# Optimization experiments

Hardware: AMD Instinct MI355X
Metric: run time of the kernel (lower is better)

Reference implementation:

```python
import jax, jax.numpy as jnp
import numpy as np

N = 50000      # nodes
E = 800000     # edges (avg degree 16)
C = 32         # channels per degree (deg0 and deg1)
HRAD = 32      # radial MLP hidden
L = 4          # attention layers (plus 1 output layer)
HEADS = 4
EPS = 1e-6
NRAD = 7 * C   # rk00, rk10, rv00, rv10, rv11, rv01, rv11b


def setup_inputs() -> dict:
    key = jax.random.key(0)
    ks = jax.random.split(key, 16)
    L1 = L + 1
    s = 0.1
    return {
        "pos": jax.random.normal(ks[0], (N, 3), jnp.float32),
        "f0": jax.random.normal(ks[1], (N, C), jnp.float32),
        "f1": jax.random.normal(ks[2], (N, C, 3), jnp.float32),
        "src": jax.random.randint(ks[3], (E,), 0, N, jnp.int32),
        "dst": jax.random.randint(ks[4], (E,), 0, N, jnp.int32),
        "W1": jax.random.normal(ks[5], (L1, 1, HRAD), jnp.float32) * s,
        "b1": jnp.zeros((L1, HRAD), jnp.float32),
        "W2": jax.random.normal(ks[6], (L1, HRAD, NRAD), jnp.float32) * s,
        "b2": jnp.zeros((L1, NRAD), jnp.float32),
        "Wq": jax.random.normal(ks[7], (L1, C, C), jnp.float32) * s,
        "Wo0": jax.random.normal(ks[8], (L1, C, C), jnp.float32) * s,
        "Wo1": jax.random.normal(ks[9], (L1, C, C), jnp.float32) * s,
        "Ws0": jax.random.normal(ks[10], (L1, C, C), jnp.float32) * s,
        "Ws1": jax.random.normal(ks[11], (L1, C, C), jnp.float32) * s,
        "bg": jnp.zeros((L, C), jnp.float32),
    }


def _attn_layer(f0, f1, u, rlen, src, dst, n, heads,
                W1, b1, W2, b2, Wq, Wo0, Wo1, Ws0, Ws1):
    # radial network, channel-wise modulation per interaction path
    h = jax.nn.relu(rlen[:, None] @ W1 + b1)            # [E, HRAD]
    R = h @ W2 + b2                                     # [E, 7C]
    rk00, rk10, rv00, rv10, rv11, rv01, rv11b = jnp.split(R, 7, axis=-1)
    f0s = f0[src]                                       # [E, C]
    f1s = f1[src]                                       # [E, C, 3]
    dot1 = jnp.einsum('ecd,ed->ec', f1s, u)             # deg1 -> invariant [E, C]
    # equivariant keys (deg0) and values (deg0 + deg1)
    k0 = rk00 * f0s + rk10 * dot1                       # [E, C]
    v0 = rv00 * f0s + rv10 * dot1                       # [E, C]
    v1 = rv11[..., None] * f1s + (rv01 * f0s + rv11b * dot1)[..., None] * u[:, None, :]  # [E, C, 3]
    # multi-head attention logits on invariants
    ch = C // heads
    q = (f0 @ Wq)[dst].reshape(-1, heads, ch)           # [E, H, ch]
    kh = k0.reshape(-1, heads, ch)
    logits = (q * kh).sum(-1) / np.sqrt(ch)             # [E, H]
    # segment softmax over incoming edges of each dst node
    m = jax.ops.segment_max(logits, dst, num_segments=n)
    e = jnp.exp(logits - m[dst])
    z = jax.ops.segment_sum(e, dst, num_segments=n)
    alpha = e / (z[dst] + EPS)                          # [E, H]
    ac = jnp.repeat(alpha, ch, axis=1)                  # [E, C]
    o0 = jax.ops.segment_sum(ac * v0, dst, num_segments=n)                  # [N, C]
    o1 = jax.ops.segment_sum(ac[..., None] * v1, dst, num_segments=n)       # [N, C, 3]
    # self-interaction + skip
    out0 = o0 @ Wo0 + f0 @ Ws0
    out1 = jnp.einsum('ncd,ce->ned', o1, Wo1) + jnp.einsum('ncd,ce->ned', f1, Ws1)
    return out0, out1


def _forward(pos, f0, f1, src, dst, W1, b1, W2, b2, Wq, Wo0, Wo1, Ws0, Ws1, bg):
    n = f0.shape[0]
    # edge-wise basis (l=0,1 spherical harmonics ~ unit direction) and radial distance
    rel = pos[dst] - pos[src]                           # [E, 3]
    rlen = jnp.linalg.norm(rel, axis=-1)                # [E]
    u = rel / (rlen + EPS)[:, None]                     # [E, 3]
    for i in range(L):
        f0, f1 = _attn_layer(f0, f1, u, rlen, src, dst, n, HEADS,
                             W1[i], b1[i], W2[i], b2[i], Wq[i],
                             Wo0[i], Wo1[i], Ws0[i], Ws1[i])
        # GProjRelu: relu on invariants, norm-gated relu on deg-1
        f0 = jax.nn.relu(f0)
        n1 = jnp.linalg.norm(f1, axis=-1)               # [N, C]
        f1 = f1 * (jax.nn.relu(n1 + bg[i]) / (n1 + EPS))[..., None]
    # final output layer: single head, no nonlinearity
    f0, f1 = _attn_layer(f0, f1, u, rlen, src, dst, n, 1,
                         W1[L], b1[L], W2[L], b2[L], Wq[L],
                         Wo0[L], Wo1[L], Ws0[L], Ws1[L])
    return f0, f1


def reference(pos, f0, f1, src, dst, W1, b1, W2, b2, Wq, Wo0, Wo1, Ws0, Ws1, bg):
    return _forward(pos, f0, f1, src, dst, W1, b1, W2, b2, Wq, Wo0, Wo1, Ws0, Ws1, bg)
```

## Files before the change

### kernel.cpp

```cpp
#include <hip/hip_runtime.h>
#include <math.h>

#define CCH 32
#define NCH 224
#define NIV 33
#define HRAD 32
#define ET 16


__global__ void hist_kernel(const int* __restrict__ dst, int* __restrict__ counts, int E) {
  int e = blockIdx.x * 256 + threadIdx.x;
  if (e < E) atomicAdd(&counts[dst[e]], 1);
}

__global__ void scan1_kernel(const int* __restrict__ counts, int* __restrict__ offs,
                             int* __restrict__ bsums, int n) {
  __shared__ int sd[1024];
  int t = threadIdx.x;
  int i = blockIdx.x * 1024 + t;
  int v = (i < n) ? counts[i] : 0;
  sd[t] = v;
  __syncthreads();
  for (int o = 1; o < 1024; o <<= 1) {
    int add = (t >= o) ? sd[t - o] : 0;
    __syncthreads();
    sd[t] += add;
    __syncthreads();
  }
  if (i < n) offs[i] = sd[t] - v;
  if (t == 1023) bsums[blockIdx.x] = sd[1023];
}

__global__ void scan2_kernel(int* bsums, int nb) {
  if (threadIdx.x == 0 && blockIdx.x == 0) {
    int acc = 0;
    for (int i = 0; i < nb; i++) { int v = bsums[i]; bsums[i] = acc; acc += v; }
  }
}

__global__ void scan3_kernel(int* __restrict__ offs, const int* __restrict__ bsums,
                             int* __restrict__ cursor, int n, int E) {
  int i = blockIdx.x * 256 + threadIdx.x;
  if (i < n) {
    int v = offs[i] + bsums[i >> 10];
    offs[i] = v;
    cursor[i] = v;
  } else if (i == n) {
    offs[n] = E;
  }
}

__global__ void scatter_kernel(const float* __restrict__ pos, const int* __restrict__ src,
                               const int* __restrict__ dst, int* __restrict__ cursor,
                               int* __restrict__ esrcS, float4* __restrict__ egeoS, int E) {
  int e = blockIdx.x * 256 + threadIdx.x;
  if (e >= E) return;
  int s = src[e], d = dst[e];
  float rx = pos[d * 3 + 0] - pos[s * 3 + 0];
  float ry = pos[d * 3 + 1] - pos[s * 3 + 1];
  float rz = pos[d * 3 + 2] - pos[s * 3 + 2];
  float rl = sqrtf(rx * rx + ry * ry + rz * rz);
  float inv = 1.0f / (rl + 1e-6f);
  int p = atomicAdd(&cursor[d], 1);
  esrcS[p] = s;
  egeoS[p] = make_float4(rx * inv, ry * inv, rz * inv, rl);
}


__global__ void pwl_build_kernel(const float* __restrict__ W1, const float* __restrict__ b1,
                                 const float* __restrict__ W2, const float* __restrict__ b2,
                                 float2* __restrict__ coef, float* __restrict__ tks) {
  int l = blockIdx.x;
  int tid = threadIdx.x;
  const float* w1 = W1 + l * HRAD;
  const float* bb1 = b1 + l * HRAD;
  const float* w2 = W2 + l * HRAD * NCH;
  const float* bb2 = b2 + l * NCH;
  __shared__ float a_s[HRAD], b_s[HRAD], t_s[HRAD], t_sorted[HRAD];
  if (tid < HRAD) {
    float a = w1[tid], b = bb1[tid];
    a_s[tid] = a; b_s[tid] = b;
    t_s[tid] = (a != 0.0f) ? (-b / a) : 1e30f;
  }
  __syncthreads();
  if (tid < HRAD) {
    float tj = t_s[tid];
    int rank = 0;
    for (int k = 0; k < HRAD; k++) {
      float tk = t_s[k];
      rank += (tk < tj) || (tk == tj && k < tid);
    }
    t_sorted[rank] = tj;
    tks[l * HRAD + tid] = tj;
  }
  __syncthreads();
  for (int idx = tid; idx < NIV * NCH; idx += blockDim.x) {
    int iv = idx / NCH;
    int k = idx - iv * NCH;
    double lo = (iv == 0) ? (double)t_sorted[0] - 1.0 : (double)t_sorted[iv - 1];
    double hi = (iv == NIV - 1) ? (double)t_sorted[HRAD - 1] + 1.0 : (double)t_sorted[iv];
    double rm = 0.5 * (lo + hi);
    if (iv == 0) rm = (double)t_sorted[0] - 1.0;
    if (iv == NIV - 1) rm = (double)t_sorted[HRAD - 1] + 1.0;
    float alpha = bb2[k];
    float beta = 0.0f;
    for (int j = 0; j < HRAD; j++) {
      if ((double)a_s[j] * rm + (double)b_s[j] > 0.0) {
        float w = w2[j * NCH + k];
        alpha = fmaf(w, b_s[j], alpha);
        beta = fmaf(w, a_s[j], beta);
      }
    }
    coef[l * (NIV * NCH) + idx] = make_float2(alpha, beta);
  }
}


__global__ __launch_bounds__(512) void pack_kernel(
    const float* __restrict__ f0, const float* __restrict__ f1,
    const float* __restrict__ Wq0, float scale0,
    float4* __restrict__ fpk, float* __restrict__ qbuf, int n) {
  __shared__ float sWq[1024];
  __shared__ float sF0[ET * 32];
  int tid = threadIdx.x;
  for (int i = tid; i < 1024; i += 512) sWq[i] = Wq0[i];
  __syncthreads();
  int nl = tid >> 5, c = tid & 31;
  for (int base = blockIdx.x * ET; base < n; base += gridDim.x * ET) {
    int node = base + nl;
    float v0 = 0.f, x = 0.f, y = 0.f, z = 0.f;
    if (node < n) {
      v0 = f0[(size_t)node * 32 + c];
      size_t b = ((size_t)node * 32 + c) * 3;
      x = f1[b]; y = f1[b + 1]; z = f1[b + 2];
      fpk[(size_t)node * 32 + c] = make_float4(v0, x, y, z);
    }
    sF0[nl * 32 + c] = v0;
    __syncthreads();
    if (node < n) {
      float q = 0.f;
#pragma unroll
      for (int k = 0; k < 32; k++) q = fmaf(sF0[nl * 32 + k], sWq[k * 32 + c], q);
      qbuf[(size_t)node * 32 + c] = q * scale0;
    }
    __syncthreads();
  }
}


__global__ __launch_bounds__(1024) void node_kernel(
    const float4* __restrict__ fpk, const float* __restrict__ qbuf,
    float4* __restrict__ Opk,
    const int* __restrict__ esrcS, const float4* __restrict__ egeoS,
    const int* __restrict__ offs,
    const float2* __restrict__ coefG, const float* __restrict__ tkG,
    int ch, int n) {
  __shared__ float2 sCoef[NIV * NCH];
  __shared__ float sTk[CCH];
  int tid = threadIdx.x;
  for (int i = tid; i < NIV * NCH; i += 1024) sCoef[i] = coefG[i];
  if (tid < CCH) sTk[tid] = tkG[tid];
  __syncthreads();

  int lane = tid & 63;
  int wid = tid >> 6;
  int c = lane & 31;
  int half = lane >> 5;
  float tk_c = sTk[c];

  for (int node = blockIdx.x * 16 + wid; node < n; node += gridDim.x * 16) {
    float qs = qbuf[(size_t)node * 32 + c];
    int start = offs[node], end = offs[node + 1];
    float m = -INFINITY, z = 0.0f;
    float o0 = 0.0f, o10 = 0.0f, o11 = 0.0f, o12 = 0.0f;

    int j = start + half;
    int sB = 0;
    float4 gA = make_float4(0, 0, 0, 0), gB = make_float4(0, 0, 0, 0);
    float4 FA = make_float4(0, 0, 0, 0);
    if (j < end) {
      int sA = esrcS[j];
      gA = egeoS[j];
      FA = fpk[(size_t)sA * 32 + c];
    }
    if (j + 2 < end) { sB = esrcS[j + 2]; gB = egeoS[j + 2]; }

    while (j < end) {
      float4 g = gA;
      float4 F = FA;
      int j2 = j + 2;
      if (j2 < end) {
        FA = fpk[(size_t)sB * 32 + c];
        gA = gB;
        if (j2 + 2 < end) { sB = esrcS[j2 + 2]; gB = egeoS[j2 + 2]; }
      }
      unsigned long long msk = __ballot(g.w > tk_c);
      int iv = half ? (int)__popcll(msk >> 32) : (int)__popcll(msk & 0xFFFFFFFFull);
      const float2* cf = sCoef + iv * NCH + c;
      float r = g.w;
      float2 q0 = cf[0],   q1 = cf[32],  q2 = cf[64], q3 = cf[96];
      float2 q4 = cf[128], q5 = cf[160], q6 = cf[192];
      float rk00 = fmaf(q0.y, r, q0.x), rk10 = fmaf(q1.y, r, q1.x);
      float rv00 = fmaf(q2.y, r, q2.x), rv10 = fmaf(q3.y, r, q3.x);
      float rv11 = fmaf(q4.y, r, q4.x), rv01 = fmaf(q5.y, r, q5.x);
      float rv11b = fmaf(q6.y, r, q6.x);
      float dot1 = fmaf(F.y, g.x, fmaf(F.z, g.y, F.w * g.z));
      float k0 = fmaf(rk00, F.x, rk10 * dot1);
      float t = qs * k0;
      for (int o = 1; o < ch; o <<= 1) t += __shfl_xor(t, o, 64);
      float mn = fmaxf(m, t);
      float a = __expf(m - mn);
      float p = __expf(t - mn);
      m = mn;
      z = fmaf(z, a, p);
      float v0 = fmaf(rv00, F.x, rv10 * dot1);
      float sg = fmaf(rv01, F.x, rv11b * dot1);
      o0  = fmaf(o0,  a, p * v0);
      o10 = fmaf(o10, a, p * fmaf(rv11, F.y, sg * g.x));
      o11 = fmaf(o11, a, p * fmaf(rv11, F.z, sg * g.y));
      o12 = fmaf(o12, a, p * fmaf(rv11, F.w, sg * g.z));
      j = j2;
    }

    float mo  = __shfl_xor(m, 32, 64);
    float zo  = __shfl_xor(z, 32, 64);
    float p0  = __shfl_xor(o0, 32, 64);
    float p10 = __shfl_xor(o10, 32, 64);
    float p11 = __shfl_xor(o11, 32, 64);
    float p12 = __shfl_xor(o12, 32, 64);
    float mf = fmaxf(m, mo);
    float aA = 0.0f, aB = 0.0f;
    if (mf > -INFINITY) { aA = __expf(m - mf); aB = __expf(mo - mf); }
    float zf = z * aA + zo * aB;
    float inv = 1.0f / (zf + 1e-6f);
    if (!half) {
      Opk[(size_t)node * 32 + c] = make_float4(
          (o0 * aA + p0 * aB) * inv,
          (o10 * aA + p10 * aB) * inv,
          (o11 * aA + p11 * aB) * inv,
          (o12 * aA + p12 * aB) * inv);
    }
  }
}


__global__ __launch_bounds__(512) void epi_kernel(
    const float4* __restrict__ Opk, float4* __restrict__ fpk,
    const float* __restrict__ Wo0G, const float* __restrict__ Ws0G,
    const float* __restrict__ Wo1G, const float* __restrict__ Ws1G,
    const float* __restrict__ bgG,
    const float* __restrict__ WqN, float* __restrict__ qbuf, float scaleN,
    float* __restrict__ out0, float* __restrict__ out1,
    int mode, int n) {
  __shared__ float4 sW[32 * 32];
  __shared__ float  sWq[32 * 32];
  __shared__ float4 sO[ET * 32];
  __shared__ float4 sF[ET * 32];
  __shared__ float  sF0[ET * 32];
  int tid = threadIdx.x;
  for (int i = tid; i < 1024; i += 512) {
    sW[i] = make_float4(Wo0G[i], Ws0G[i], Wo1G[i], Ws1G[i]);
    if (mode == 0) sWq[i] = WqN[i];
  }
  __syncthreads();
  int nl = tid >> 5;
  int c  = tid & 31;
  for (int base = blockIdx.x * ET; base < n; base += gridDim.x * ET) {
    int node = base + nl;
    bool valid = node < n;
    {
      int gn = base + (tid >> 5);
      if (gn < n) {
        sO[tid] = Opk[(size_t)gn * 32 + (tid & 31)];
        sF[tid] = fpk[(size_t)gn * 32 + (tid & 31)];
      }
    }
    __syncthreads();
    float a0 = 0.f, ax = 0.f, ay = 0.f, az = 0.f;
#pragma unroll
    for (int k = 0; k < 32; k++) {
      float4 O = sO[nl * 32 + k];
      float4 F = sF[nl * 32 + k];
      float4 w = sW[k * 32 + c];
      a0 = fmaf(O.x, w.x, fmaf(F.x, w.y, a0));
      ax = fmaf(O.y, w.z, fmaf(F.y, w.w, ax));
      ay = fmaf(O.z, w.z, fmaf(F.z, w.w, ay));
      az = fmaf(O.w, w.z, fmaf(F.w, w.w, az));
    }
    if (mode == 0) {
      float f0n = fmaxf(a0, 0.f);
      float n1 = sqrtf(fmaf(ax, ax, fmaf(ay, ay, az * az)));
      float gate = fmaxf(n1 + bgG[c], 0.f) / (n1 + 1e-6f);
      if (valid) fpk[(size_t)node * 32 + c] = make_float4(f0n, ax * gate, ay * gate, az * gate);
      sF0[nl * 32 + c] = f0n;
      __syncthreads();
      if (valid) {
        float q = 0.f;
#pragma unroll
        for (int k = 0; k < 32; k++) q = fmaf(sF0[nl * 32 + k], sWq[k * 32 + c], q);
        qbuf[(size_t)node * 32 + c] = q * scaleN;
      }
      __syncthreads();
    } else {
      if (valid) {
        out0[(size_t)node * 32 + c] = a0;
        size_t b = ((size_t)node * 32 + c) * 3;
        out1[b] = ax; out1[b + 1] = ay; out1[b + 2] = az;
      }
      __syncthreads();
    }
  }
}


extern "C" void kernel_launch(void* const* d_in, const int* in_sizes, int n_in,
                              void* d_out, int out_size, void* d_ws, size_t ws_size,
                              hipStream_t stream) {
  const float* pos = (const float*)d_in[0];
  const float* f0  = (const float*)d_in[1];
  const float* f1  = (const float*)d_in[2];
  const int* src   = (const int*)d_in[3];
  const int* dst   = (const int*)d_in[4];
  const float* W1  = (const float*)d_in[5];
  const float* b1  = (const float*)d_in[6];
  const float* W2  = (const float*)d_in[7];
  const float* b2  = (const float*)d_in[8];
  const float* Wq  = (const float*)d_in[9];
  const float* Wo0 = (const float*)d_in[10];
  const float* Wo1 = (const float*)d_in[11];
  const float* Ws0 = (const float*)d_in[12];
  const float* Ws1 = (const float*)d_in[13];
  const float* bg  = (const float*)d_in[14];

  int N = in_sizes[0] / 3;
  int E = in_sizes[3];

  char* p = (char*)d_ws;
  auto alloc = [&](size_t bytes) {
    char* r = p;
    p += (bytes + 255) & ~(size_t)255;
    return r;
  };
  int* counts   = (int*)alloc((size_t)N * 4);
  int* offs     = (int*)alloc((size_t)(N + 1) * 4);
  int* cursor   = (int*)alloc((size_t)N * 4);
  int* bsums    = (int*)alloc(1024 * 4);
  int* esrcS    = (int*)alloc((size_t)E * 4);
  float4* egeoS = (float4*)alloc((size_t)E * 16);
  float2* coef  = (float2*)alloc((size_t)5 * NIV * NCH * 8);
  float* tks    = (float*)alloc((size_t)5 * HRAD * 4);
  float4* fpk   = (float4*)alloc((size_t)N * CCH * 16);
  float4* Opk   = (float4*)alloc((size_t)N * CCH * 16);
  float* qbuf   = (float*)alloc((size_t)N * CCH * 4);

  hipMemsetAsync(counts, 0, (size_t)N * 4, stream);
  hist_kernel<<<(E + 255) / 256, 256, 0, stream>>>(dst, counts, E);
  int nb = (N + 1023) / 1024;
  scan1_kernel<<<nb, 1024, 0, stream>>>(counts, offs, bsums, N);
  scan2_kernel<<<1, 64, 0, stream>>>(bsums, nb);
  scan3_kernel<<<(N + 1 + 255) / 256, 256, 0, stream>>>(offs, bsums, cursor, N, E);
  scatter_kernel<<<(E + 255) / 256, 256, 0, stream>>>(pos, src, dst, cursor, esrcS, egeoS, E);
  pwl_build_kernel<<<5, 256, 0, stream>>>(W1, b1, W2, b2, coef, tks);

  float sc8 = 1.0f / sqrtf(8.0f);
  float sc32 = 1.0f / sqrtf(32.0f);
  pack_kernel<<<512, 512, 0, stream>>>(f0, f1, Wq, sc8, fpk, qbuf, N);

  float* out0 = (float*)d_out;
  float* out1 = out0 + (size_t)N * CCH;
  for (int l = 0; l < 5; l++) {
    bool last = (l == 4);
    int ch = last ? 32 : 8;
    node_kernel<<<512, 1024, 0, stream>>>(
        fpk, qbuf, Opk, esrcS, egeoS, offs,
        coef + (size_t)l * NIV * NCH, tks + l * HRAD, ch, N);
    epi_kernel<<<512, 512, 0, stream>>>(
        Opk, fpk,
        Wo0 + l * CCH * CCH, Ws0 + l * CCH * CCH,
        Wo1 + l * CCH * CCH, Ws1 + l * CCH * CCH,
        bg + (last ? 0 : l) * CCH,
        Wq + (l + 1 <= 4 ? (l + 1) : 4) * CCH * CCH, qbuf,
        (l + 1 == 4) ? sc32 : sc8,
        out0, out1, last ? 1 : 0, N);
  }
}
```

Before: 889.6 us.

## Precompute per-layer PWL interval indices per edge; template head reduction width

The scatter kernel now computes, once for each edge, the piecewise-linear interval index for all five layers by counting knots below the edge length. It packs the five 6-bit indices into an int alongside the source index, stored as an int2 per edge. The node kernel reads the packed index instead of doing a ballot and popcount per edge, and is templated on the head channel count so the shuffle reduction unrolls. Other edits switch size_t indexing to int, simplify the epilogue loads, and move the PWL build ahead of the scatter. The cost is 4 extra bytes per edge of traffic in every layer.

```diff
diff --git a/kernel.cpp b/kernel.cpp
--- a/kernel.cpp
+++ b/kernel.cpp
@@ -52,8 +52,13 @@
 
 __global__ void scatter_kernel(const float* __restrict__ pos, const int* __restrict__ src,
                                const int* __restrict__ dst, int* __restrict__ cursor,
-                               int* __restrict__ esrcS, float4* __restrict__ egeoS, int E) {
-  int e = blockIdx.x * 256 + threadIdx.x;
+                               const float* __restrict__ tks,
+                               int2* __restrict__ eidx, float4* __restrict__ egeoS, int E) {
+  __shared__ float stk[5 * HRAD];
+  int tid = threadIdx.x;
+  if (tid < 5 * HRAD) stk[tid] = tks[tid];
+  __syncthreads();
+  int e = blockIdx.x * 256 + tid;
   if (e >= E) return;
   int s = src[e], d = dst[e];
   float rx = pos[d * 3 + 0] - pos[s * 3 + 0];
@@ -61,8 +66,16 @@
   float rz = pos[d * 3 + 2] - pos[s * 3 + 2];
   float rl = sqrtf(rx * rx + ry * ry + rz * rz);
   float inv = 1.0f / (rl + 1e-6f);
+  int pk = 0;
+#pragma unroll
+  for (int l = 0; l < 5; l++) {
+    int cnt = 0;
+#pragma unroll
+    for (int k = 0; k < HRAD; k++) cnt += (rl > stk[l * HRAD + k]) ? 1 : 0;
+    pk |= cnt << (6 * l);
+  }
   int p = atomicAdd(&cursor[d], 1);
-  esrcS[p] = s;
+  eidx[p] = make_int2(s, pk);
   egeoS[p] = make_float4(rx * inv, ry * inv, rz * inv, rl);
 }
 
@@ -130,10 +143,10 @@
     int node = base + nl;
     float v0 = 0.f, x = 0.f, y = 0.f, z = 0.f;
     if (node < n) {
-      v0 = f0[(size_t)node * 32 + c];
-      size_t b = ((size_t)node * 32 + c) * 3;
+      v0 = f0[node * 32 + c];
+      int b = (node * 32 + c) * 3;
       x = f1[b]; y = f1[b + 1]; z = f1[b + 2];
-      fpk[(size_t)node * 32 + c] = make_float4(v0, x, y, z);
+      fpk[node * 32 + c] = make_float4(v0, x, y, z);
     }
     sF0[nl * 32 + c] = v0;
     __syncthreads();
@@ -141,61 +154,59 @@
       float q = 0.f;
 #pragma unroll
       for (int k = 0; k < 32; k++) q = fmaf(sF0[nl * 32 + k], sWq[k * 32 + c], q);
-      qbuf[(size_t)node * 32 + c] = q * scale0;
+      qbuf[node * 32 + c] = q * scale0;
     }
     __syncthreads();
   }
 }
 
 
+template <int CH>
 __global__ __launch_bounds__(1024) void node_kernel(
     const float4* __restrict__ fpk, const float* __restrict__ qbuf,
     float4* __restrict__ Opk,
-    const int* __restrict__ esrcS, const float4* __restrict__ egeoS,
+    const int2* __restrict__ eidx, const float4* __restrict__ egeoS,
     const int* __restrict__ offs,
-    const float2* __restrict__ coefG, const float* __restrict__ tkG,
-    int ch, int n) {
+    const float2* __restrict__ coefG,
+    int shift, int n) {
   __shared__ float2 sCoef[NIV * NCH];
-  __shared__ float sTk[CCH];
   int tid = threadIdx.x;
   for (int i = tid; i < NIV * NCH; i += 1024) sCoef[i] = coefG[i];
-  if (tid < CCH) sTk[tid] = tkG[tid];
   __syncthreads();
 
   int lane = tid & 63;
   int wid = tid >> 6;
   int c = lane & 31;
   int half = lane >> 5;
-  float tk_c = sTk[c];
 
   for (int node = blockIdx.x * 16 + wid; node < n; node += gridDim.x * 16) {
-    float qs = qbuf[(size_t)node * 32 + c];
+    float qs = qbuf[node * 32 + c];
     int start = offs[node], end = offs[node + 1];
     float m = -INFINITY, z = 0.0f;
     float o0 = 0.0f, o10 = 0.0f, o11 = 0.0f, o12 = 0.0f;
 
     int j = start + half;
-    int sB = 0;
+    int2 eA = make_int2(0, 0), eB = make_int2(0, 0);
     float4 gA = make_float4(0, 0, 0, 0), gB = make_float4(0, 0, 0, 0);
     float4 FA = make_float4(0, 0, 0, 0);
     if (j < end) {
-      int sA = esrcS[j];
+      eA = eidx[j];
       gA = egeoS[j];
-      FA = fpk[(size_t)sA * 32 + c];
-    }
-    if (j + 2 < end) { sB = esrcS[j + 2]; gB = egeoS[j + 2]; }
+      FA = fpk[eA.x * 32 + c];
+    }
+    if (j + 2 < end) { eB = eidx[j + 2]; gB = egeoS[j + 2]; }
 
     while (j < end) {
       float4 g = gA;
       float4 F = FA;
+      int ivw = eA.y;
       int j2 = j + 2;
       if (j2 < end) {
-        FA = fpk[(size_t)sB * 32 + c];
-        gA = gB;
-        if (j2 + 2 < end) { sB = esrcS[j2 + 2]; gB = egeoS[j2 + 2]; }
+        FA = fpk[eB.x * 32 + c];
+        gA = gB; eA = eB;
+        if (j2 + 2 < end) { eB = eidx[j2 + 2]; gB = egeoS[j2 + 2]; }
       }
-      unsigned long long msk = __ballot(g.w > tk_c);
-      int iv = half ? (int)__popcll(msk >> 32) : (int)__popcll(msk & 0xFFFFFFFFull);
+      int iv = (ivw >> shift) & 63;
       const float2* cf = sCoef + iv * NCH + c;
       float r = g.w;
       float2 q0 = cf[0],   q1 = cf[32],  q2 = cf[64], q3 = cf[96];
@@ -207,7 +218,8 @@
       float dot1 = fmaf(F.y, g.x, fmaf(F.z, g.y, F.w * g.z));
       float k0 = fmaf(rk00, F.x, rk10 * dot1);
       float t = qs * k0;
-      for (int o = 1; o < ch; o <<= 1) t += __shfl_xor(t, o, 64);
+#pragma unroll
+      for (int o = 1; o < CH; o <<= 1) t += __shfl_xor(t, o, 64);
       float mn = fmaxf(m, t);
       float a = __expf(m - mn);
       float p = __expf(t - mn);
@@ -234,7 +246,7 @@
     float zf = z * aA + zo * aB;
     float inv = 1.0f / (zf + 1e-6f);
     if (!half) {
-      Opk[(size_t)node * 32 + c] = make_float4(
+      Opk[node * 32 + c] = make_float4(
           (o0 * aA + p0 * aB) * inv,
           (o10 * aA + p10 * aB) * inv,
           (o11 * aA + p11 * aB) * inv,
@@ -268,12 +280,9 @@
   for (int base = blockIdx.x * ET; base < n; base += gridDim.x * ET) {
     int node = base + nl;
     bool valid = node < n;
-    {
-      int gn = base + (tid >> 5);
-      if (gn < n) {
-        sO[tid] = Opk[(size_t)gn * 32 + (tid & 31)];
-        sF[tid] = fpk[(size_t)gn * 32 + (tid & 31)];
-      }
+    if (valid) {
+      sO[tid] = Opk[node * 32 + c];
+      sF[tid] = fpk[node * 32 + c];
     }
     __syncthreads();
     float a0 = 0.f, ax = 0.f, ay = 0.f, az = 0.f;
@@ -291,20 +300,20 @@
       float f0n = fmaxf(a0, 0.f);
       float n1 = sqrtf(fmaf(ax, ax, fmaf(ay, ay, az * az)));
       float gate = fmaxf(n1 + bgG[c], 0.f) / (n1 + 1e-6f);
-      if (valid) fpk[(size_t)node * 32 + c] = make_float4(f0n, ax * gate, ay * gate, az * gate);
+      if (valid) fpk[node * 32 + c] = make_float4(f0n, ax * gate, ay * gate, az * gate);
       sF0[nl * 32 + c] = f0n;
       __syncthreads();
       if (valid) {
         float q = 0.f;
 #pragma unroll
         for (int k = 0; k < 32; k++) q = fmaf(sF0[nl * 32 + k], sWq[k * 32 + c], q);
-        qbuf[(size_t)node * 32 + c] = q * scaleN;
+        qbuf[node * 32 + c] = q * scaleN;
       }
       __syncthreads();
     } else {
       if (valid) {
-        out0[(size_t)node * 32 + c] = a0;
-        size_t b = ((size_t)node * 32 + c) * 3;
+        out0[node * 32 + c] = a0;
+        int b = (node * 32 + c) * 3;
         out1[b] = ax; out1[b + 1] = ay; out1[b + 2] = az;
       }
       __syncthreads();
@@ -345,7 +354,7 @@
   int* offs     = (int*)alloc((size_t)(N + 1) * 4);
   int* cursor   = (int*)alloc((size_t)N * 4);
   int* bsums    = (int*)alloc(1024 * 4);
-  int* esrcS    = (int*)alloc((size_t)E * 4);
+  int2* eidx    = (int2*)alloc((size_t)E * 8);
   float4* egeoS = (float4*)alloc((size_t)E * 16);
   float2* coef  = (float2*)alloc((size_t)5 * NIV * NCH * 8);
   float* tks    = (float*)alloc((size_t)5 * HRAD * 4);
@@ -353,14 +362,14 @@
   float4* Opk   = (float4*)alloc((size_t)N * CCH * 16);
   float* qbuf   = (float*)alloc((size_t)N * CCH * 4);
 
+  pwl_build_kernel<<<5, 256, 0, stream>>>(W1, b1, W2, b2, coef, tks);
   hipMemsetAsync(counts, 0, (size_t)N * 4, stream);
   hist_kernel<<<(E + 255) / 256, 256, 0, stream>>>(dst, counts, E);
   int nb = (N + 1023) / 1024;
   scan1_kernel<<<nb, 1024, 0, stream>>>(counts, offs, bsums, N);
   scan2_kernel<<<1, 64, 0, stream>>>(bsums, nb);
   scan3_kernel<<<(N + 1 + 255) / 256, 256, 0, stream>>>(offs, bsums, cursor, N, E);
-  scatter_kernel<<<(E + 255) / 256, 256, 0, stream>>>(pos, src, dst, cursor, esrcS, egeoS, E);
-  pwl_build_kernel<<<5, 256, 0, stream>>>(W1, b1, W2, b2, coef, tks);
+  scatter_kernel<<<(E + 255) / 256, 256, 0, stream>>>(pos, src, dst, cursor, tks, eidx, egeoS, E);
 
   float sc8 = 1.0f / sqrtf(8.0f);
   float sc32 = 1.0f / sqrtf(32.0f);
@@ -370,10 +379,15 @@
   float* out1 = out0 + (size_t)N * CCH;
   for (int l = 0; l < 5; l++) {
     bool last = (l == 4);
-    int ch = last ? 32 : 8;
-    node_kernel<<<512, 1024, 0, stream>>>(
-        fpk, qbuf, Opk, esrcS, egeoS, offs,
-        coef + (size_t)l * NIV * NCH, tks + l * HRAD, ch, N);
+    if (last) {
+      node_kernel<32><<<512, 1024, 0, stream>>>(
+          fpk, qbuf, Opk, eidx, egeoS, offs,
+          coef + (size_t)l * NIV * NCH, 6 * l, N);
+    } else {
+      node_kernel<8><<<512, 1024, 0, stream>>>(
+          fpk, qbuf, Opk, eidx, egeoS, offs,
+          coef + (size_t)l * NIV * NCH, 6 * l, N);
+    }
     epi_kernel<<<512, 512, 0, stream>>>(
         Opk, fpk,
         Wo0 + l * CCH * CCH, Ws0 + l * CCH * CCH,
```

After: 941.9 us. +5.9%, slower.
